# Kernel optimization log

Measured on AMD Instinct MI355X. Metric: run time of the kernel, lower is better.

## Reference

```python
import jax, jax.numpy as jnp
import numpy as np

N_QUBITS = 8
N_WORDS = 16
DEGREE = 3
N_ANSATZ_LAYERS = 2
VOCAB = 50257
EMB = 512
BATCH = 16
N_ROTS = 4 * N_QUBITS * N_ANSATZ_LAYERS  # 64
DIM = 2 ** N_QUBITS


def _ry_mat(th):
    # [[cos, -sin],[sin, cos]] on theta/2, batched over leading dim
    c = jnp.cos(th / 2).astype(jnp.complex64)
    s = jnp.sin(th / 2).astype(jnp.complex64)
    return jnp.stack([jnp.stack([c, -s], -1), jnp.stack([s, c], -1)], -2)


def _rx_mat(th):
    # [[cos, -i sin],[-i sin, cos]] on theta/2
    c = jnp.cos(th / 2).astype(jnp.complex64)
    s = jnp.sin(th / 2).astype(jnp.complex64)
    return jnp.stack([jnp.stack([c, -1j * s], -1), jnp.stack([-1j * s, c], -1)], -2)


def _apply_1q(st, M, w):
    # st: [BB, 2^n] complex, M: [BB,2,2]; wire 0 is the most-significant axis (tq convention)
    BB = st.shape[0]
    s = st.reshape(BB, 2 ** w, 2, -1)
    s = jnp.einsum('bij,bljr->blir', M, s)
    return s.reshape(BB, -1)


def _apply_ctrl(st, M, c, t, n):
    # controlled-1q gate: apply M on target t only in the control=1 subspace
    BB = st.shape[0]
    full = st.reshape((BB,) + (2,) * n)
    s0 = jnp.take(full, 0, axis=c + 1)
    s1 = jnp.take(full, 1, axis=c + 1)
    ta = (t if t < c else t - 1) + 1  # target axis after removing control axis
    s1 = jnp.moveaxis(s1, ta, -1)
    s1 = jnp.einsum('bij,b...j->b...i', M, s1)
    s1 = jnp.moveaxis(s1, -1, ta)
    return jnp.stack([s0, s1], axis=c + 1).reshape(BB, -1)


def _sim14(st, params, n, layers):
    # circuit-14 ansatz: ry ring, crx down-ring, ry ring, crx up-ring (per layer)
    idx = 0
    for _ in range(layers):
        for i in range(n):
            st = _apply_1q(st, _ry_mat(params[:, idx]), i); idx += 1
        for i in range(n - 1, -1, -1):
            st = _apply_ctrl(st, _rx_mat(params[:, idx]), i, (i + 1) % n, n); idx += 1
        for i in range(n):
            st = _apply_1q(st, _ry_mat(params[:, idx]), i); idx += 1
        for i in [n - 1] + list(range(n - 1)):
            st = _apply_ctrl(st, _rx_mat(params[:, idx]), i, (i - 1) % n, n); idx += 1
    return st


def _apply_unitaries(base, wparams, coeffs):
    # base: [B, DIM]; wparams: [B, W, N_ROTS]; coeffs: [B, W] complex -> LCU sum_w c_w U_w |psi>
    B, W = wparams.shape[0], wparams.shape[1]
    rep = jnp.repeat(base, W, axis=0)  # matches torch repeat(1,W).view(-1,DIM)
    st = _sim14(rep, wparams.reshape(B * W, -1), N_QUBITS, N_ANSATZ_LAYERS)
    return jnp.einsum('bwi,bw->bi', st.reshape(B, W, DIM), coeffs)


def _measure_xyz(st, n):
    # Pauli X/Y/Z expectations per wire; order: [x_0..x_{n-1}, y_..., z_...]
    BB = st.shape[0]
    xs, ys, zs = [], [], []
    for w in range(n):
        s = st.reshape(BB, 2 ** w, 2, -1)
        a0, a1 = s[:, :, 0, :], s[:, :, 1, :]
        cross = jnp.sum(jnp.conj(a0) * a1, axis=(1, 2))
        xs.append(2 * jnp.real(cross))
        ys.append(2 * jnp.imag(cross))
        zs.append(jnp.sum(jnp.abs(a0) ** 2 - jnp.abs(a1) ** 2, axis=(1, 2)))
    return jnp.concatenate([jnp.stack(xs, -1), jnp.stack(ys, -1), jnp.stack(zs, -1)], axis=-1)


def reference(x, embedding_W, emb2rot_W, emb2rot_b, poly_coeffs, mix_coeffs_ri, qff_params, ff1_W, ff1_b, ff2_W, ff2_b):
    B = x.shape[0]
    mix = (mix_coeffs_ri[:, 0] + 1j * mix_coeffs_ri[:, 1]).astype(jnp.complex64)
    coeffs = mix / jnp.maximum(jnp.sum(jnp.abs(mix)), 1e-12)  # L1 normalize
    coeffs = jnp.broadcast_to(coeffs[None, :], (B, N_WORDS))
    emb = embedding_W[x]                       # [B, W, EMB]
    wparams = emb @ emb2rot_W.T + emb2rot_b    # [B, W, N_ROTS]; dropout is identity in eval
    base = jnp.zeros((B, DIM), jnp.complex64).at[:, 0].set(1.0)
    acc = poly_coeffs[0] * base
    work = base
    for d in range(1, DEGREE + 1):
        work = _apply_unitaries(work, wparams, coeffs)
        acc = acc + poly_coeffs[d] * work
    mixed = acc / jnp.sum(jnp.abs(poly_coeffs))
    final_probs = jnp.linalg.norm(mixed, axis=-1)
    normed = mixed / jnp.maximum(final_probs, 1e-12)[:, None]
    qp = jnp.broadcast_to(qff_params[None, :4 * N_QUBITS], (B, 4 * N_QUBITS))  # qff uses 1 layer
    st = _sim14(normed, qp, N_QUBITS, 1)
    exps = _measure_xyz(st, N_QUBITS)          # [B, 3*n_qubits]
    h = jax.nn.relu(exps @ ff1_W.T + ff1_b)
    op = h @ ff2_W.T + ff2_b
    return op, jnp.mean(final_probs)


def setup_inputs():
    key = jax.random.key(0)
    ks = jax.random.split(key, 12)
    x = jax.random.randint(ks[0], (BATCH, N_WORDS), 0, VOCAB)
    embedding_W = jax.random.normal(ks[1], (VOCAB, EMB), jnp.float32) * 0.02
    emb2rot_W = jax.random.normal(ks[2], (N_ROTS, EMB), jnp.float32) * (1.0 / np.sqrt(EMB))
    emb2rot_b = jax.random.normal(ks[3], (N_ROTS,), jnp.float32) * 0.01
    poly_coeffs = jax.random.uniform(ks[4], (DEGREE + 1,), jnp.float32)
    mix_coeffs_ri = jax.random.uniform(ks[5], (N_WORDS, 2), jnp.float32)
    qff_params = jax.random.uniform(ks[6], (N_ROTS,), jnp.float32)
    NM = 3 * N_QUBITS
    ff1_W = jax.random.normal(ks[7], (EMB, NM), jnp.float32) * (1.0 / np.sqrt(NM))
    ff1_b = jnp.zeros((EMB,), jnp.float32)
    ff2_W = jax.random.normal(ks[8], (VOCAB, EMB), jnp.float32) * (1.0 / np.sqrt(EMB))
    ff2_b = jnp.zeros((VOCAB,), jnp.float32)
    return {"x": x, "embedding_W": embedding_W, "emb2rot_W": emb2rot_W, "emb2rot_b": emb2rot_b,
            "poly_coeffs": poly_coeffs, "mix_coeffs_ri": mix_coeffs_ri, "qff_params": qff_params,
            "ff1_W": ff1_W, "ff1_b": ff1_b, "ff2_W": ff2_W, "ff2_b": ff2_b}
```

## Files before the change

### kernel.cpp

```cpp
#include <hip/hip_runtime.h>
#include <hip/hip_bf16.h>

#define NQ 8
#define DIM 256
#define NB 16
#define NW 16
#define VOCABN 50257
#define EMBN 512

__device__ __forceinline__ float2 shfl2(float2 a, int m){
  float2 r; r.x = __shfl_xor(a.x, m, 64); r.y = __shfl_xor(a.y, m, 64); return r;
}
__device__ __forceinline__ float wave_sum(float x){
  #pragma unroll
  for (int off = 1; off < 64; off <<= 1) x += __shfl_xor(x, off, 64);
  return x;
}

__device__ __forceinline__ void ry_pair(float2& a0, float2& a1, float c, float s){
  float2 n0 = make_float2(c*a0.x - s*a1.x, c*a0.y - s*a1.y);
  float2 n1 = make_float2(s*a0.x + c*a1.x, s*a0.y + c*a1.y);
  a0 = n0; a1 = n1;
}
__device__ __forceinline__ void rx_pair(float2& a0, float2& a1, float c, float s){
  float2 n0 = make_float2(c*a0.x + s*a1.y, c*a0.y - s*a1.x);
  float2 n1 = make_float2(c*a1.x + s*a0.y, c*a1.y - s*a0.x);
  a0 = n0; a1 = n1;
}

__device__ __forceinline__ void apply_gate(float2 v[4], int lane, int kind, int cbit, int tbit,
                                           float c, float s){
  if (kind == 0){
    if (tbit == 7){ ry_pair(v[0], v[2], c, s); ry_pair(v[1], v[3], c, s); }
    else if (tbit == 6){ ry_pair(v[0], v[1], c, s); ry_pair(v[2], v[3], c, s); }
    else {
      int m = 1 << tbit;
      #pragma unroll
      for (int r = 0; r < 4; ++r){
        float2 w = shfl2(v[r], m);
        float sg = (lane & m) ? s : -s;
        v[r] = make_float2(c*v[r].x + sg*w.x, c*v[r].y + sg*w.y);
      }
    }
  } else {
    if (tbit >= 6){
      if (cbit >= 6){
        if (cbit == 7) rx_pair(v[2], v[3], c, s);
        else           rx_pair(v[1], v[3], c, s);
      } else {
        int cm = 1 << cbit;
        if (lane & cm){
          if (tbit == 7){ rx_pair(v[0], v[2], c, s); rx_pair(v[1], v[3], c, s); }
          else          { rx_pair(v[0], v[1], c, s); rx_pair(v[2], v[3], c, s); }
        }
      }
    } else {
      int m = 1 << tbit;
      if (cbit >= 6){
        int r0 = (cbit == 6) ? 1 : 2;
        float2 w0 = shfl2(v[r0], m);
        float2 w1 = shfl2(v[3], m);
        v[r0] = make_float2(c*v[r0].x + s*w0.y, c*v[r0].y - s*w0.x);
        v[3]  = make_float2(c*v[3].x  + s*w1.y, c*v[3].y  - s*w1.x);
      } else {
        int cm = 1 << cbit;
        bool act = (lane & cm) != 0;
        #pragma unroll
        for (int r = 0; r < 4; ++r){
          float2 w = shfl2(v[r], m);
          if (act) v[r] = make_float2(c*v[r].x + s*w.y, c*v[r].y - s*w.x);
        }
      }
    }
  }
}

__device__ __forceinline__ void sim32(float2 v[4], int lane, const float2* __restrict__ cs){
  constexpr int KIND[32] = {0,0,0,0,0,0,0,0, 1,1,1,1,1,1,1,1, 0,0,0,0,0,0,0,0, 1,1,1,1,1,1,1,1};
  constexpr int CB[32]   = {0,0,0,0,0,0,0,0, 0,1,2,3,4,5,6,7, 0,0,0,0,0,0,0,0, 0,7,6,5,4,3,2,1};
  constexpr int TB[32]   = {7,6,5,4,3,2,1,0, 7,0,1,2,3,4,5,6, 7,6,5,4,3,2,1,0, 1,0,7,6,5,4,3,2};
  #pragma unroll
  for (int g = 0; g < 32; ++g){
    float2 p = cs[g];
    apply_gate(v, lane, KIND[g], CB[g], TB[g], p.x, p.y);
  }
}

__device__ __forceinline__ void measure_one(const float2 v[4], int lane, int t,
                                            float& xr, float& xi, float& zz){
  xr = 0.f; xi = 0.f; zz = 0.f;
  if (t == 7){
    #pragma unroll
    for (int r = 0; r < 2; ++r){
      float2 a0 = v[r], a1 = v[r+2];
      xr += a0.x*a1.x + a0.y*a1.y;
      xi += a0.x*a1.y - a0.y*a1.x;
      zz += (a0.x*a0.x + a0.y*a0.y) - (a1.x*a1.x + a1.y*a1.y);
    }
  } else if (t == 6){
    #pragma unroll
    for (int r = 0; r < 4; r += 2){
      float2 a0 = v[r], a1 = v[r+1];
      xr += a0.x*a1.x + a0.y*a1.y;
      xi += a0.x*a1.y - a0.y*a1.x;
      zz += (a0.x*a0.x + a0.y*a0.y) - (a1.x*a1.x + a1.y*a1.y);
    }
  } else {
    int m = 1 << t;
    #pragma unroll
    for (int r = 0; r < 4; ++r){
      float2 a = v[r];
      float2 w = shfl2(a, m);
      if (!(lane & m)){
        xr += a.x*w.x + a.y*w.y;
        xi += a.x*w.y - a.y*w.x;
        zz += (a.x*a.x + a.y*a.y) - (w.x*w.x + w.y*w.y);
      }
    }
  }
  xr = wave_sum(xr); xi = wave_sum(xi); zz = wave_sum(zz);
}

__global__ __launch_bounds__(64) void k_prep(
    const int* __restrict__ x, const float* __restrict__ embW,
    const float* __restrict__ e2rW, const float* __restrict__ e2rb,
    const float* __restrict__ mixri, const float* __restrict__ qff,
    float* __restrict__ wcs, float* __restrict__ coeffs, float* __restrict__ qcs)
{
  const int p = blockIdx.x;
  const int j = threadIdx.x;
  const int tok = x[p];
  const float4* er = (const float4*)(embW + (size_t)tok * EMBN);
  const float4* wr = (const float4*)(e2rW + (size_t)j * EMBN);
  float acc = e2rb[j];
  #pragma unroll 4
  for (int k = 0; k < EMBN/4; ++k){
    float4 e = er[k], w4 = wr[k];
    acc += e.x*w4.x + e.y*w4.y + e.z*w4.z + e.w*w4.w;
  }
  float th = 0.5f * acc;
  wcs[(p*64 + j)*2 + 0] = cosf(th);
  wcs[(p*64 + j)*2 + 1] = sinf(th);
  if (p == 0){
    if (j < 32){ float t = 0.5f * qff[j]; qcs[2*j] = cosf(t); qcs[2*j+1] = sinf(t); }
    if (j < 16){
      float ssum = 0.f;
      for (int i = 0; i < 16; ++i){
        float mr = mixri[2*i], mi = mixri[2*i+1];
        ssum += sqrtf(mr*mr + mi*mi);
      }
      ssum = fmaxf(ssum, 1e-12f);
      coeffs[2*j]   = mixri[2*j]   / ssum;
      coeffs[2*j+1] = mixri[2*j+1] / ssum;
    }
  }
}

__global__ __launch_bounds__(1024) void k_sim(
    const float* __restrict__ wcs, const float* __restrict__ coeffs,
    const float* __restrict__ qcs, const float* __restrict__ poly,
    const float* __restrict__ ff1W, const float* __restrict__ ff1b,
    float* __restrict__ hT, float* __restrict__ fprobs)
{
  const int b = blockIdx.x;
  const int tid = threadIdx.x;
  const int w = tid >> 6;
  const int lane = tid & 63;

  __shared__ float2 wcs_s[NW*64];
  __shared__ float2 qcs_s[32];
  __shared__ float2 stall[NW][DIM];
  __shared__ float2 partial[4][DIM];
  __shared__ float2 work[DIM];
  __shared__ float2 accs[DIM];
  __shared__ float  exps[24];
  __shared__ float  inv_s;
  __shared__ float  ff1_lds[EMBN*24];

  wcs_s[tid] = ((const float2*)wcs)[b*(NW*64) + tid];
  if (tid < 32) qcs_s[tid] = ((const float2*)qcs)[tid];
  {
    const float4* f4 = (const float4*)ff1W;
    float4* d4 = (float4*)ff1_lds;
    #pragma unroll
    for (int i = 0; i < 3; ++i) d4[i*1024 + tid] = f4[i*1024 + tid];
  }
  if (tid < DIM){
    float p0 = poly[0];
    float one = (tid == 0) ? 1.f : 0.f;
    work[tid] = make_float2(one, 0.f);
    accs[tid] = make_float2(p0*one, 0.f);
  }
  __syncthreads();

  const float2 coef = make_float2(coeffs[2*w], coeffs[2*w+1]);
  const float2* mycs = &wcs_s[w*64];

  for (int d = 1; d <= 3; ++d){
    float2 v[4];
    #pragma unroll
    for (int r = 0; r < 4; ++r) v[r] = work[(r<<6) | lane];
    for (int l = 0; l < 2; ++l) sim32(v, lane, mycs + 32*l);
    #pragma unroll
    for (int r = 0; r < 4; ++r){
      float2 a = v[r];
      stall[w][(r<<6) | lane] = make_float2(coef.x*a.x - coef.y*a.y, coef.x*a.y + coef.y*a.x);
    }
    __syncthreads();
    {
      int idx = tid & 255, grp = tid >> 8;
      float2 s = make_float2(0.f, 0.f);
      #pragma unroll
      for (int ww = 0; ww < 4; ++ww){
        float2 a = stall[grp*4 + ww][idx];
        s.x += a.x; s.y += a.y;
      }
      partial[grp][idx] = s;
    }
    __syncthreads();
    if (tid < DIM){
      float2 s = make_float2(0.f, 0.f);
      #pragma unroll
      for (int g2 = 0; g2 < 4; ++g2){ s.x += partial[g2][tid].x; s.y += partial[g2][tid].y; }
      float pd = poly[d];
      work[tid] = s;
      accs[tid].x += pd*s.x; accs[tid].y += pd*s.y;
    }
    __syncthreads();
  }

  const float psum = fabsf(poly[0]) + fabsf(poly[1]) + fabsf(poly[2]) + fabsf(poly[3]);
  if (tid < DIM){
    work[tid] = make_float2(accs[tid].x/psum, accs[tid].y/psum);
  }
  __syncthreads();

  if (w == 0){
    float ss = 0.f;
    #pragma unroll
    for (int r = 0; r < 4; ++r){
      float2 m = work[(r<<6) | lane];
      ss += m.x*m.x + m.y*m.y;
    }
    ss = wave_sum(ss);
    float fp = sqrtf(ss);
    if (lane == 0){
      fprobs[b] = fp;
      inv_s = 1.f / fmaxf(fp, 1e-12f);
    }
  }
  __syncthreads();

  if (w < 8){
    float inv = inv_s;
    float2 v[4];
    #pragma unroll
    for (int r = 0; r < 4; ++r){
      float2 m = work[(r<<6) | lane];
      v[r] = make_float2(m.x*inv, m.y*inv);
    }
    sim32(v, lane, &qcs_s[0]);
    float xr, xi, zz;
    measure_one(v, lane, 7 - w, xr, xi, zz);
    if (lane == 0){ exps[w] = 2.f*xr; exps[8+w] = 2.f*xi; exps[16+w] = zz; }
  }
  __syncthreads();

  if (tid < EMBN){
    float a = ff1b[tid];
    const float* wr = ff1_lds + tid*24;
    #pragma unroll
    for (int m2 = 0; m2 < 24; ++m2) a += exps[m2]*wr[m2];
    a = fmaxf(a, 0.f);
    hT[tid*NB + b] = a;
  }
}

__global__ __launch_bounds__(256) void k_out(
    const float* __restrict__ hT, const float* __restrict__ ff2W,
    const float* __restrict__ ff2b, const float* __restrict__ fprobs,
    float* __restrict__ out)
{
  __shared__ float4 smem[2048];
  const int tid = threadIdx.x;

  if (blockIdx.x == 0 && tid == 0){
    float s = 0.f;
    #pragma unroll
    for (int i = 0; i < 16; ++i) s += fprobs[i];
    out[(size_t)NB*VOCABN] = s * (1.f/16.f);
  }

  {
    const float4* hT4 = (const float4*)hT;
    #pragma unroll
    for (int i = 0; i < 8; ++i) smem[i*256 + tid] = hT4[i*256 + tid];
  }
  __syncthreads();

  const int rrow = tid & 127;
  const int half = tid >> 7;
  const int row  = blockIdx.x * 128 + rrow;
  const bool valid = (row < VOCABN);

  float4 a0 = make_float4(0,0,0,0), a1 = a0, a2 = a0, a3 = a0;

  if (valid){
    const float4* wv = (const float4*)(ff2W + (size_t)row * EMBN) + half*64;
    const int kbase = half*256;
    #pragma unroll 8
    for (int c = 0; c < 64; ++c){
      float4 wq = wv[c];
      const int k0 = (kbase + c*4) << 2;
      float4 h00 = smem[k0+0],  h01 = smem[k0+1],  h02 = smem[k0+2],  h03 = smem[k0+3];
      float4 h10 = smem[k0+4],  h11 = smem[k0+5],  h12 = smem[k0+6],  h13 = smem[k0+7];
      float4 h20 = smem[k0+8],  h21 = smem[k0+9],  h22 = smem[k0+10], h23 = smem[k0+11];
      float4 h30 = smem[k0+12], h31 = smem[k0+13], h32 = smem[k0+14], h33 = smem[k0+15];
      a0.x += wq.x*h00.x + wq.y*h10.x + wq.z*h20.x + wq.w*h30.x;
      a0.y += wq.x*h00.y + wq.y*h10.y + wq.z*h20.y + wq.w*h30.y;
      a0.z += wq.x*h00.z + wq.y*h10.z + wq.z*h20.z + wq.w*h30.z;
      a0.w += wq.x*h00.w + wq.y*h10.w + wq.z*h20.w + wq.w*h30.w;
      a1.x += wq.x*h01.x + wq.y*h11.x + wq.z*h21.x + wq.w*h31.x;
      a1.y += wq.x*h01.y + wq.y*h11.y + wq.z*h21.y + wq.w*h31.y;
      a1.z += wq.x*h01.z + wq.y*h11.z + wq.z*h21.z + wq.w*h31.z;
      a1.w += wq.x*h01.w + wq.y*h11.w + wq.z*h21.w + wq.w*h31.w;
      a2.x += wq.x*h02.x + wq.y*h12.x + wq.z*h22.x + wq.w*h32.x;
      a2.y += wq.x*h02.y + wq.y*h12.y + wq.z*h22.y + wq.w*h32.y;
      a2.z += wq.x*h02.z + wq.y*h12.z + wq.z*h22.z + wq.w*h32.z;
      a2.w += wq.x*h02.w + wq.y*h12.w + wq.z*h22.w + wq.w*h32.w;
      a3.x += wq.x*h03.x + wq.y*h13.x + wq.z*h23.x + wq.w*h33.x;
      a3.y += wq.x*h03.y + wq.y*h13.y + wq.z*h23.y + wq.w*h33.y;
      a3.z += wq.x*h03.z + wq.y*h13.z + wq.z*h23.z + wq.w*h33.z;
      a3.w += wq.x*h03.w + wq.y*h13.w + wq.z*h23.w + wq.w*h33.w;
    }
  }
  __syncthreads();

  if (half == 1){
    smem[0*128 + rrow] = a0;
    smem[1*128 + rrow] = a1;
    smem[2*128 + rrow] = a2;
    smem[3*128 + rrow] = a3;
  }
  __syncthreads();
  if (half == 0 && valid){
    float4 b0 = smem[0*128 + rrow], b1 = smem[1*128 + rrow];
    float4 b2 = smem[2*128 + rrow], b3 = smem[3*128 + rrow];
    a0.x += b0.x; a0.y += b0.y; a0.z += b0.z; a0.w += b0.w;
    a1.x += b1.x; a1.y += b1.y; a1.z += b1.z; a1.w += b1.w;
    a2.x += b2.x; a2.y += b2.y; a2.z += b2.z; a2.w += b2.w;
    a3.x += b3.x; a3.y += b3.y; a3.z += b3.z; a3.w += b3.w;
    const float bias = ff2b[row];
    out[(size_t) 0*VOCABN + row] = a0.x + bias;
    out[(size_t) 1*VOCABN + row] = a0.y + bias;
    out[(size_t) 2*VOCABN + row] = a0.z + bias;
    out[(size_t) 3*VOCABN + row] = a0.w + bias;
    out[(size_t) 4*VOCABN + row] = a1.x + bias;
    out[(size_t) 5*VOCABN + row] = a1.y + bias;
    out[(size_t) 6*VOCABN + row] = a1.z + bias;
    out[(size_t) 7*VOCABN + row] = a1.w + bias;
    out[(size_t) 8*VOCABN + row] = a2.x + bias;
    out[(size_t) 9*VOCABN + row] = a2.y + bias;
    out[(size_t)10*VOCABN + row] = a2.z + bias;
    out[(size_t)11*VOCABN + row] = a2.w + bias;
    out[(size_t)12*VOCABN + row] = a3.x + bias;
    out[(size_t)13*VOCABN + row] = a3.y + bias;
    out[(size_t)14*VOCABN + row] = a3.z + bias;
    out[(size_t)15*VOCABN + row] = a3.w + bias;
  }
}

extern "C" void kernel_launch(void* const* d_in, const int* in_sizes, int n_in,
                              void* d_out, int out_size, void* d_ws, size_t ws_size,
                              hipStream_t stream)
{
  const int*   x     = (const int*)  d_in[0];
  const float* embW  = (const float*)d_in[1];
  const float* e2rW  = (const float*)d_in[2];
  const float* e2rb  = (const float*)d_in[3];
  const float* poly  = (const float*)d_in[4];
  const float* mixri = (const float*)d_in[5];
  const float* qff   = (const float*)d_in[6];
  const float* ff1W  = (const float*)d_in[7];
  const float* ff1b  = (const float*)d_in[8];
  const float* ff2W  = (const float*)d_in[9];
  const float* ff2b  = (const float*)d_in[10];
  float* out = (float*)d_out;
  float* ws  = (float*)d_ws;

  float* wcs    = ws;
  float* coeffs = ws + 32768;
  float* qcs    = ws + 32800;
  float* hT     = ws + 32864;
  float* fprobs = ws + 41056;

  k_prep<<<256, 64, 0, stream>>>(x, embW, e2rW, e2rb, mixri, qff, wcs, coeffs, qcs);
  k_sim <<<NB, 1024, 0, stream>>>(wcs, coeffs, qcs, poly, ff1W, ff1b, hT, fprobs);
  k_out <<<(VOCABN + 127)/128, 256, 0, stream>>>(hT, ff2W, ff2b, fprobs, out);
}
```

Measured before the change: 301.2 us.

## Split quantum simulation across many small blocks and narrow output GEMV rows

The single 16-block simulation kernel becomes a chain of kernels: one 64-thread block per (batch, word) pair runs the circuit, and the reduction over words goes through global memory between polynomial degrees. A final kernel sums the last degree, normalises, measures and applies ff1. The aim is to replace a 16-block, heavily synchronised kernel with 256 parallel blocks, at the cost of extra launches and global round-trips. The output GEMV also moves from 128 rows per block split in two K-halves to 64 rows per block split in four K-quarters, giving more blocks and shorter per-thread loops.

```diff
diff --git a/kernel.cpp b/kernel.cpp
--- a/kernel.cpp
+++ b/kernel.cpp
@@ -156,124 +156,130 @@
   }
 }
 
-__global__ __launch_bounds__(1024) void k_sim(
+__global__ __launch_bounds__(64) void k_deg1(
     const float* __restrict__ wcs, const float* __restrict__ coeffs,
-    const float* __restrict__ qcs, const float* __restrict__ poly,
+    float2* __restrict__ S1)
+{
+  const int p = blockIdx.x, lane = threadIdx.x;
+  const float2* mycs = ((const float2*)wcs) + p*64;
+  float2 v[4];
+  v[0] = make_float2(lane == 0 ? 1.f : 0.f, 0.f);
+  v[1] = v[2] = v[3] = make_float2(0.f, 0.f);
+  sim32(v, lane, mycs);
+  sim32(v, lane, mycs + 32);
+  const float2 coef = ((const float2*)coeffs)[p & 15];
+  #pragma unroll
+  for (int r = 0; r < 4; ++r){
+    float2 a = v[r];
+    S1[p*DIM + ((r<<6) | lane)] = make_float2(coef.x*a.x - coef.y*a.y, coef.x*a.y + coef.y*a.x);
+  }
+}
+
+__global__ __launch_bounds__(64) void k_deg(
+    const float2* __restrict__ Sin, float2* __restrict__ Sout,
+    const float* __restrict__ wcs, const float* __restrict__ coeffs,
+    const float* __restrict__ poly, float2* __restrict__ accs, int dprev)
+{
+  const int p = blockIdx.x, lane = threadIdx.x;
+  const int b = p >> 4, w = p & 15;
+  float2 v[4];
+  v[0] = v[1] = v[2] = v[3] = make_float2(0.f, 0.f);
+  const float2* base = Sin + b*NW*DIM;
+  #pragma unroll
+  for (int ww = 0; ww < NW; ++ww){
+    #pragma unroll
+    for (int r = 0; r < 4; ++r){
+      float2 a = base[ww*DIM + ((r<<6) | lane)];
+      v[r].x += a.x; v[r].y += a.y;
+    }
+  }
+  if (w == 0){
+    const float pd = poly[dprev];
+    #pragma unroll
+    for (int r = 0; r < 4; ++r){
+      const int idx = (r<<6) | lane;
+      float2 cur = make_float2(pd*v[r].x, pd*v[r].y);
+      if (dprev == 1){
+        if (idx == 0) cur.x += poly[0];
+        accs[b*DIM + idx] = cur;
+      } else {
+        float2 old = accs[b*DIM + idx];
+        accs[b*DIM + idx] = make_float2(old.x + cur.x, old.y + cur.y);
+      }
+    }
+  }
+  const float2* mycs = ((const float2*)wcs) + p*64;
+  sim32(v, lane, mycs);
+  sim32(v, lane, mycs + 32);
+  const float2 coef = ((const float2*)coeffs)[w];
+  #pragma unroll
+  for (int r = 0; r < 4; ++r){
+    float2 a = v[r];
+    Sout[p*DIM + ((r<<6) | lane)] = make_float2(coef.x*a.x - coef.y*a.y, coef.x*a.y + coef.y*a.x);
+  }
+}
+
+__global__ __launch_bounds__(512) void k_final(
+    const float2* __restrict__ Sin, const float2* __restrict__ accs,
+    const float* __restrict__ poly, const float* __restrict__ qcs,
     const float* __restrict__ ff1W, const float* __restrict__ ff1b,
     float* __restrict__ hT, float* __restrict__ fprobs)
 {
-  const int b = blockIdx.x;
-  const int tid = threadIdx.x;
-  const int w = tid >> 6;
-  const int lane = tid & 63;
-
-  __shared__ float2 wcs_s[NW*64];
-  __shared__ float2 qcs_s[32];
-  __shared__ float2 stall[NW][DIM];
-  __shared__ float2 partial[4][DIM];
+  const int b = blockIdx.x, tid = threadIdx.x;
+  const int w = tid >> 6, lane = tid & 63;
   __shared__ float2 work[DIM];
-  __shared__ float2 accs[DIM];
+  __shared__ float  red[8];
   __shared__ float  exps[24];
   __shared__ float  inv_s;
   __shared__ float  ff1_lds[EMBN*24];
 
-  wcs_s[tid] = ((const float2*)wcs)[b*(NW*64) + tid];
-  if (tid < 32) qcs_s[tid] = ((const float2*)qcs)[tid];
   {
     const float4* f4 = (const float4*)ff1W;
     float4* d4 = (float4*)ff1_lds;
     #pragma unroll
-    for (int i = 0; i < 3; ++i) d4[i*1024 + tid] = f4[i*1024 + tid];
-  }
+    for (int i = 0; i < 6; ++i) d4[i*512 + tid] = f4[i*512 + tid];
+  }
+  const float psum = fabsf(poly[0]) + fabsf(poly[1]) + fabsf(poly[2]) + fabsf(poly[3]);
+  float ssl = 0.f;
   if (tid < DIM){
-    float p0 = poly[0];
-    float one = (tid == 0) ? 1.f : 0.f;
-    work[tid] = make_float2(one, 0.f);
-    accs[tid] = make_float2(p0*one, 0.f);
-  }
-  __syncthreads();
-
-  const float2 coef = make_float2(coeffs[2*w], coeffs[2*w+1]);
-  const float2* mycs = &wcs_s[w*64];
-
-  for (int d = 1; d <= 3; ++d){
-    float2 v[4];
-    #pragma unroll
-    for (int r = 0; r < 4; ++r) v[r] = work[(r<<6) | lane];
-    for (int l = 0; l < 2; ++l) sim32(v, lane, mycs + 32*l);
-    #pragma unroll
-    for (int r = 0; r < 4; ++r){
-      float2 a = v[r];
-      stall[w][(r<<6) | lane] = make_float2(coef.x*a.x - coef.y*a.y, coef.x*a.y + coef.y*a.x);
-    }
-    __syncthreads();
-    {
-      int idx = tid & 255, grp = tid >> 8;
-      float2 s = make_float2(0.f, 0.f);
-      #pragma unroll
-      for (int ww = 0; ww < 4; ++ww){
-        float2 a = stall[grp*4 + ww][idx];
-        s.x += a.x; s.y += a.y;
-      }
-      partial[grp][idx] = s;
-    }
-    __syncthreads();
-    if (tid < DIM){
-      float2 s = make_float2(0.f, 0.f);
-      #pragma unroll
-      for (int g2 = 0; g2 < 4; ++g2){ s.x += partial[g2][tid].x; s.y += partial[g2][tid].y; }
-      float pd = poly[d];
-      work[tid] = s;
-      accs[tid].x += pd*s.x; accs[tid].y += pd*s.y;
-    }
-    __syncthreads();
-  }
-
-  const float psum = fabsf(poly[0]) + fabsf(poly[1]) + fabsf(poly[2]) + fabsf(poly[3]);
-  if (tid < DIM){
-    work[tid] = make_float2(accs[tid].x/psum, accs[tid].y/psum);
-  }
-  __syncthreads();
-
-  if (w == 0){
-    float ss = 0.f;
-    #pragma unroll
-    for (int r = 0; r < 4; ++r){
-      float2 m = work[(r<<6) | lane];
-      ss += m.x*m.x + m.y*m.y;
-    }
-    ss = wave_sum(ss);
-    float fp = sqrtf(ss);
-    if (lane == 0){
-      fprobs[b] = fp;
-      inv_s = 1.f / fmaxf(fp, 1e-12f);
-    }
-  }
-  __syncthreads();
-
-  if (w < 8){
-    float inv = inv_s;
+    float2 s = make_float2(0.f, 0.f);
+    const float2* base = Sin + b*NW*DIM;
+    #pragma unroll
+    for (int ww = 0; ww < NW; ++ww){ float2 a = base[ww*DIM + tid]; s.x += a.x; s.y += a.y; }
+    float2 ac = accs[b*DIM + tid];
+    const float p3 = poly[3];
+    s = make_float2((ac.x + p3*s.x)/psum, (ac.y + p3*s.y)/psum);
+    work[tid] = s;
+    ssl = s.x*s.x + s.y*s.y;
+  }
+  ssl = wave_sum(ssl);
+  if (lane == 0) red[w] = ssl;
+  __syncthreads();
+  if (tid == 0){
+    float fp = sqrtf(red[0] + red[1] + red[2] + red[3]);
+    fprobs[b] = fp;
+    inv_s = 1.f / fmaxf(fp, 1e-12f);
+  }
+  __syncthreads();
+  {
+    const float inv = inv_s;
     float2 v[4];
     #pragma unroll
     for (int r = 0; r < 4; ++r){
       float2 m = work[(r<<6) | lane];
       v[r] = make_float2(m.x*inv, m.y*inv);
     }
-    sim32(v, lane, &qcs_s[0]);
+    sim32(v, lane, (const float2*)qcs);
     float xr, xi, zz;
     measure_one(v, lane, 7 - w, xr, xi, zz);
     if (lane == 0){ exps[w] = 2.f*xr; exps[8+w] = 2.f*xi; exps[16+w] = zz; }
   }
   __syncthreads();
-
-  if (tid < EMBN){
-    float a = ff1b[tid];
-    const float* wr = ff1_lds + tid*24;
-    #pragma unroll
-    for (int m2 = 0; m2 < 24; ++m2) a += exps[m2]*wr[m2];
-    a = fmaxf(a, 0.f);
-    hT[tid*NB + b] = a;
-  }
+  float a = ff1b[tid];
+  const float* wr = ff1_lds + tid*24;
+  #pragma unroll
+  for (int m2 = 0; m2 < 24; ++m2) a += exps[m2]*wr[m2];
+  hT[tid*NB + b] = fmaxf(a, 0.f);
 }
 
 __global__ __launch_bounds__(256) void k_out(
@@ -298,18 +304,18 @@
   }
   __syncthreads();
 
-  const int rrow = tid & 127;
-  const int half = tid >> 7;
-  const int row  = blockIdx.x * 128 + rrow;
+  const int r = tid & 63;
+  const int q = tid >> 6;
+  const int row = blockIdx.x*64 + r;
   const bool valid = (row < VOCABN);
 
   float4 a0 = make_float4(0,0,0,0), a1 = a0, a2 = a0, a3 = a0;
 
   if (valid){
-    const float4* wv = (const float4*)(ff2W + (size_t)row * EMBN) + half*64;
-    const int kbase = half*256;
+    const float4* wv = (const float4*)(ff2W + (size_t)row * EMBN) + q*32;
+    const int kbase = q*128;
     #pragma unroll 8
-    for (int c = 0; c < 64; ++c){
+    for (int c = 0; c < 32; ++c){
       float4 wq = wv[c];
       const int k0 = (kbase + c*4) << 2;
       float4 h00 = smem[k0+0],  h01 = smem[k0+1],  h02 = smem[k0+2],  h03 = smem[k0+3];
@@ -336,20 +342,23 @@
   }
   __syncthreads();
 
-  if (half == 1){
-    smem[0*128 + rrow] = a0;
-    smem[1*128 + rrow] = a1;
-    smem[2*128 + rrow] = a2;
-    smem[3*128 + rrow] = a3;
-  }
-  __syncthreads();
-  if (half == 0 && valid){
-    float4 b0 = smem[0*128 + rrow], b1 = smem[1*128 + rrow];
-    float4 b2 = smem[2*128 + rrow], b3 = smem[3*128 + rrow];
-    a0.x += b0.x; a0.y += b0.y; a0.z += b0.z; a0.w += b0.w;
-    a1.x += b1.x; a1.y += b1.y; a1.z += b1.z; a1.w += b1.w;
-    a2.x += b2.x; a2.y += b2.y; a2.z += b2.z; a2.w += b2.w;
-    a3.x += b3.x; a3.y += b3.y; a3.z += b3.z; a3.w += b3.w;
+  if (q > 0){
+    smem[0*256 + q*64 + r] = a0;
+    smem[1*256 + q*64 + r] = a1;
+    smem[2*256 + q*64 + r] = a2;
+    smem[3*256 + q*64 + r] = a3;
+  }
+  __syncthreads();
+  if (q == 0 && valid){
+    #pragma unroll
+    for (int qq = 1; qq < 4; ++qq){
+      float4 b0 = smem[0*256 + qq*64 + r], b1 = smem[1*256 + qq*64 + r];
+      float4 b2 = smem[2*256 + qq*64 + r], b3 = smem[3*256 + qq*64 + r];
+      a0.x += b0.x; a0.y += b0.y; a0.z += b0.z; a0.w += b0.w;
+      a1.x += b1.x; a1.y += b1.y; a1.z += b1.z; a1.w += b1.w;
+      a2.x += b2.x; a2.y += b2.y; a2.z += b2.z; a2.w += b2.w;
+      a3.x += b3.x; a3.y += b3.y; a3.z += b3.z; a3.w += b3.w;
+    }
     const float bias = ff2b[row];
     out[(size_t) 0*VOCABN + row] = a0.x + bias;
     out[(size_t) 1*VOCABN + row] = a0.y + bias;
@@ -388,13 +397,19 @@
   float* out = (float*)d_out;
   float* ws  = (float*)d_ws;
 
-  float* wcs    = ws;
-  float* coeffs = ws + 32768;
-  float* qcs    = ws + 32800;
-  float* hT     = ws + 32864;
-  float* fprobs = ws + 41056;
-
-  k_prep<<<256, 64, 0, stream>>>(x, embW, e2rW, e2rb, mixri, qff, wcs, coeffs, qcs);
-  k_sim <<<NB, 1024, 0, stream>>>(wcs, coeffs, qcs, poly, ff1W, ff1b, hT, fprobs);
-  k_out <<<(VOCABN + 127)/128, 256, 0, stream>>>(hT, ff2W, ff2b, fprobs, out);
-}
+  float*  wcs    = ws;
+  float*  coeffs = ws + 32768;
+  float*  qcs    = ws + 32800;
+  float*  hT     = ws + 32864;
+  float*  fprobs = ws + 41056;
+  float2* accs   = (float2*)(ws + 41072);
+  float2* S1     = (float2*)(ws + 49264);
+  float2* S2     = (float2*)(ws + 180336);
+
+  k_prep <<<256, 64, 0, stream>>>(x, embW, e2rW, e2rb, mixri, qff, wcs, coeffs, qcs);
+  k_deg1 <<<256, 64, 0, stream>>>(wcs, coeffs, S1);
+  k_deg  <<<256, 64, 0, stream>>>(S1, S2, wcs, coeffs, poly, accs, 1);
+  k_deg  <<<256, 64, 0, stream>>>(S2, S1, wcs, coeffs, poly, accs, 2);
+  k_final<<<NB, 512, 0, stream>>>(S1, accs, poly, qcs, ff1W, ff1b, hT, fprobs);
+  k_out  <<<(VOCABN + 63)/64, 256, 0, stream>>>(hT, ff2W, ff2b, fprobs, out);
+}
```

After: 289.2 us. -4.0%, faster.
